# Kernel tuning notes

Hardware: AMD Instinct MI355X
Metric: run time of the kernel (lower is better)

The kernel has to match this reference:

```python
import jax, jax.numpy as jnp
import numpy as np

N = 80         # max_num_nodes
ITERS = 50     # mpm max_iters


def setup_inputs() -> dict:
    key = jax.random.key(0)
    k1, k2 = jax.random.split(key)
    # reconstructed (predicted) adjacency probabilities, kept strictly in (0,1) for BCE
    recon = jax.random.uniform(k1, (N, N), jnp.float32) * 0.98 + 0.01
    # ground-truth binary adjacency, symmetric with self-loops (adj[i,i] used in S build)
    adj = (jax.random.uniform(k2, (N, N), jnp.float32) > 0.5).astype(jnp.float32)
    adj = jnp.maximum(adj, adj.T)
    adj = adj.at[jnp.arange(N), jnp.arange(N)].set(1.0)
    return {"recon_grf": recon, "original_grf": adj}


def _forward(recon, adj):
    # degree-like matching features
    out_features = jnp.sum(recon, axis=1)   # recon node features g_a
    adj_features = jnp.sum(adj, axis=1)     # original node features f_i

    adj_d = jnp.diagonal(adj)               # adj[i,i]
    rec_d = jnp.diagonal(recon)             # recon[a,a]
    eye = jnp.eye(N, dtype=recon.dtype)
    off = 1.0 - eye

    # off-diagonal edge affinities (zero when i==j or a==b, matching the loop skips)
    src = adj * adj_d[:, None] * adj_d[None, :] * off     # [i,j] = adj[i,j]*adj[i,i]*adj[j,j]
    tgt = recon * rec_d[:, None] * rec_d[None, :] * off   # [a,b] = recon[a,b]*recon[a,a]*recon[b,b]

    # diagonal affinities S[i,i,a,a] = adj[i,i]*recon[a,a]*sim(f_i, g_a)
    sim = 1.0 / (jnp.abs(adj_features[:, None] - out_features[None, :]) + 1.0)  # [i,a]
    d = adj_d[:, None] * rec_d[None, :] * sim                                   # [i,a]

    # full affinity tensor S[i,j,a,b]  (N^4 elements)
    S = src[:, :, None, None] * tgt[None, None, :, :] \
        + (eye[:, :, None, None] * eye[None, None, :, :]) * d[:, None, :, None]

    # max-pooling matching (mpm), 50 iterations; checkpoint keeps vjp memory at 1 iter
    @jax.checkpoint
    def step(x):
        # pooled[i,j,a] = max_b x[j,b] * S[i,j,a,b]
        pooled = jnp.max(x[None, :, None, :] * S, axis=3)     # [i,j,a]
        neigh = jnp.sum(pooled * off[:, :, None], axis=1)     # sum over j != i -> [i,a]
        x_new = x * d + neigh                                 # d[i,a] == S[i,i,a,a]
        return x_new / jnp.linalg.norm(x_new)

    x0 = jnp.full((N, N), 1.0 / N, dtype=recon.dtype)
    assignment, _ = jax.lax.scan(lambda x, _: (step(x), None), x0, None, length=ITERS)

    # BCE on the upper triangle (incl. diagonal), mean reduction like F.binary_cross_entropy
    iu = jnp.triu_indices(N)
    t = adj[iu]
    p = recon[iu]
    loss = -jnp.mean(t * jnp.log(p) + (1.0 - t) * jnp.log(1.0 - p))
    return loss, assignment


def reference(recon_grf, original_grf):
    return _forward(recon_grf, original_grf)
```

## Files before the change

### kernel.cpp

```cpp
#include <hip/hip_runtime.h>
#include <math.h>

#define NN 80
#define MITERS 50
#define NTHREADS 1024

typedef _Float16 h8 __attribute__((ext_vector_type(8)));
typedef float f4 __attribute__((ext_vector_type(4)));

__device__ __forceinline__ unsigned pk_mul_f16(unsigned a, unsigned b) {
  unsigned d; asm("v_pk_mul_f16 %0, %1, %2" : "=v"(d) : "v"(a), "v"(b)); return d;
}
__device__ __forceinline__ unsigned pk_max_f16(unsigned a, unsigned b) {
  unsigned d; asm("v_pk_max_f16 %0, %1, %2" : "=v"(d) : "v"(a), "v"(b)); return d;
}
__device__ __forceinline__ h8 as_h8(uint4 u) {
  union { uint4 u; h8 h; } x; x.u = u; return x.h;
}

#define OFF_XH    0
#define OFF_TT    13120
#define OFF_MM0   26240
#define OFF_MM1   42880
#define OFF_SRCH  59520
#define OFF_DLT   76160
#define OFF_FR    103040
#define OFF_FA    103360
#define OFF_RD    103680
#define OFF_AD    104000
#define OFF_WSUM  104320
#define OFF_LSUM  104448
#define LDS_BYTES 104512

#define PB(r, k) ((((r) >> 2) * 656) + (((k) >> 1) * 16) + (((r) & 3) * 4) + (((k) & 1) * 2))

#define DO_TILE(I0, A0, AF)                                                   \
  {                                                                           \
    f4 acc = {0.f, 0.f, 0.f, 0.f};                                            \
    _Pragma("unroll")                                                         \
    for (int ks = 0; ks < 3; ++ks) {                                          \
      const int mo = ((A0) + la) * 208 + ks * 64 + gr * 16;                   \
      const uint4 b0 = *(const uint4*)(MM0b + mo);                            \
      const uint4 b1 = *(const uint4*)(MM1b + mo);                            \
      uint4 bb;                                                               \
      bb.x = pk_max_f16(b0.x, b1.x); bb.y = pk_max_f16(b0.y, b1.y);           \
      bb.z = pk_max_f16(b0.z, b1.z); bb.w = pk_max_f16(b0.w, b1.w);           \
      acc = __builtin_amdgcn_mfma_f32_16x16x32_f16(as_h8(AF[ks]),             \
                                                   as_h8(bb), acc, 0, 0, 0);  \
    }                                                                         \
    const int col = (A0) + la;                                                \
    const int rb = (I0) + gr * 4;                                             \
    const float4 dl = *(const float4*)(DLTb + col * 336 + rb * 4);            \
    char* xa = XHb + (rb >> 2) * 656 + (col >> 1) * 16 + (col & 1) * 2;       \
    const float xo0 = (float)*(const _Float16*)(xa);                          \
    const float xo1 = (float)*(const _Float16*)(xa + 4);                      \
    const float xo2 = (float)*(const _Float16*)(xa + 8);                      \
    const float xo3 = (float)*(const _Float16*)(xa + 12);                     \
    const float n0 = fmaf(xo0, dl.x, acc[0]) * inv;                           \
    const float n1 = fmaf(xo1, dl.y, acc[1]) * inv;                           \
    const float n2 = fmaf(xo2, dl.z, acc[2]) * inv;                           \
    const float n3 = fmaf(xo3, dl.w, acc[3]) * inv;                           \
    ss += n0 * n0 + n1 * n1 + n2 * n2 + n3 * n3;                              \
    *(_Float16*)(xa) = (_Float16)n0;                                          \
    *(_Float16*)(xa + 4) = (_Float16)n1;                                      \
    *(_Float16*)(xa + 8) = (_Float16)n2;                                      \
    *(_Float16*)(xa + 12) = (_Float16)n3;                                     \
  }

__global__ void __launch_bounds__(NTHREADS)
grf_kernel(const float* __restrict__ recon, const float* __restrict__ adj,
           float* __restrict__ out) {
  extern __shared__ char ldsb[];
  char* XHb = ldsb + OFF_XH;
  char* TTb = ldsb + OFF_TT;
  char* MM0b = ldsb + OFF_MM0;
  char* MM1b = ldsb + OFF_MM1;
  char* SRCHb = ldsb + OFF_SRCH;
  char* DLTb = ldsb + OFF_DLT;
  float* FR = (float*)(ldsb + OFF_FR);
  float* FA = (float*)(ldsb + OFF_FA);
  float* RD = (float*)(ldsb + OFF_RD);
  float* AD = (float*)(ldsb + OFF_AD);
  float* WSUM = (float*)(ldsb + OFF_WSUM);
  float* LSUM = (float*)(ldsb + OFF_LSUM);

  const int t = threadIdx.x;
  const int wave = t >> 6, lane = t & 63;
  const int la = lane & 15, gr = lane >> 4;

  if (t < 80) {
    float s = 0.f;
    for (int b = 0; b < NN; ++b) s += recon[t * NN + b];
    FR[t] = s;
    RD[t] = recon[t * NN + t];
  } else if (t < 160) {
    const int i = t - 80;
    float s = 0.f;
    for (int j = 0; j < NN; ++j) s += adj[i * NN + j];
    FA[i] = s;
    AD[i] = adj[i * NN + i];
  }
  if (t < 32) {
    const float q = (float)(_Float16)(1.0f / 80.0f);
    WSUM[t] = (t == 0) ? 6400.0f * q * q : 0.f;
  }
  __syncthreads();

  float lacc = 0.f;
  for (int f = t; f < NN * NN; f += NTHREADS) {
    const int r = f / NN, c = f - (f / NN) * NN;
    *(_Float16*)(XHb + PB(r, c)) = (_Float16)(1.0f / 80.0f);
    const float tv = (r == c) ? 0.f : recon[r * NN + c] * RD[r] * RD[c];
    *(_Float16*)(TTb + PB(r, c)) = (_Float16)tv;
    *(float*)(DLTb + (c * 84 + r) * 4) =
        AD[r] * RD[c] / (fabsf(FA[r] - FR[c]) + 1.f);
    const float sv = (r == c) ? 0.f : adj[r * NN + c] * AD[r] * AD[c];
    *(_Float16*)(SRCHb + (r * 104 + c) * 2) = (_Float16)sv;
    if (c >= r) {
      const float tb = adj[f], p = recon[f];
      lacc -= tb * logf(p) + (1.f - tb) * logf(1.f - p);
    }
  }
  for (int f = t; f < 1920; f += NTHREADS) {
    const int r = f / 24, j = 80 + (f - (f / 24) * 24);
    *(_Float16*)(SRCHb + (r * 104 + j) * 2) = (_Float16)0.f;
  }
  for (int f = t; f < 8320; f += NTHREADS) *(unsigned*)(MM0b + f * 4) = 0u;

  #pragma unroll
  for (int off = 32; off > 0; off >>= 1) lacc += __shfl_down(lacc, off, 64);
  if (lane == 0) LSUM[wave] = lacc;
  __syncthreads();
  if (t == 0) {
    float s = 0.f;
    for (int w = 0; w < 16; ++w) s += LSUM[w];
    out[0] = s / 3240.f;
  }

  const int i00 = (wave / 5) * 16, a00 = (wave % 5) * 16;
  const int tt1 = wave + 16;
  const bool has2 = tt1 < 25;
  const int i01 = has2 ? (tt1 / 5) * 16 : 0;
  const int a01 = has2 ? (tt1 % 5) * 16 : 0;
  uint4 af0[3], af1[3];
  af1[0] = af1[1] = af1[2] = make_uint4(0u, 0u, 0u, 0u);
  #pragma unroll
  for (int ks = 0; ks < 3; ++ks)
    af0[ks] = *(const uint4*)(SRCHb + (i00 + la) * 208 + ks * 64 + gr * 16);
  if (has2) {
    #pragma unroll
    for (int ks = 0; ks < 3; ++ks)
      af1[ks] = *(const uint4*)(SRCHb + (i01 + la) * 208 + ks * 64 + gr * 16);
  }

  const bool actA = t < 800;
  const int g = (t >= 400) ? 1 : 0;
  const int u = g ? t - 400 : t;
  const int rtA = u / 20, ctA = u - (u / 20) * 20;
  const char* xAp = XHb + rtA * 656 + g * 320;
  const char* tAp = TTb + ctA * 656 + g * 320;
  char* mwp = (g ? MM1b : MM0b) + ctA * 4 * 208 + rtA * 8;

  for (int it = 0; it < MITERS; ++it) {
    if (actA) {
      unsigned m[4][4] = {{0u, 0u, 0u, 0u}, {0u, 0u, 0u, 0u},
                          {0u, 0u, 0u, 0u}, {0u, 0u, 0u, 0u}};
      #pragma unroll 4
      for (int cc = 0; cc < 20; ++cc) {
        const uint4 xq = *(const uint4*)(xAp + cc * 16);
        const uint4 tq = *(const uint4*)(tAp + cc * 16);
        const unsigned xr[4] = {xq.x, xq.y, xq.z, xq.w};
        const unsigned tc[4] = {tq.x, tq.y, tq.z, tq.w};
        #pragma unroll
        for (int r = 0; r < 4; ++r)
          #pragma unroll
          for (int c = 0; c < 4; ++c)
            m[r][c] = pk_max_f16(m[r][c], pk_mul_f16(xr[r], tc[c]));
      }
      #pragma unroll
      for (int c = 0; c < 4; ++c) {
        unsigned fr[4];
        #pragma unroll
        for (int r = 0; r < 4; ++r) {
          const unsigned v = m[r][c];
          fr[r] = pk_max_f16(v, (v >> 16) | (v << 16));
        }
        const unsigned w0 = (fr[0] & 0xffffu) | (fr[1] << 16);
        const unsigned w1 = (fr[2] & 0xffffu) | (fr[3] << 16);
        *(uint2*)(mwp + c * 208) = make_uint2(w0, w1);
      }
    }
    __syncthreads();

    const float* WIN = WSUM + ((it & 1) << 4);
    const float4 wa = *(const float4*)(WIN);
    const float4 wb = *(const float4*)(WIN + 4);
    const float4 wc = *(const float4*)(WIN + 8);
    const float4 wd = *(const float4*)(WIN + 12);
    const float tot = ((wa.x + wa.y) + (wa.z + wa.w)) +
                      ((wb.x + wb.y) + (wb.z + wb.w)) +
                      ((wc.x + wc.y) + (wc.z + wc.w)) +
                      ((wd.x + wd.y) + (wd.z + wd.w));
    const float inv = 1.0f / sqrtf(tot);

    float ss = 0.f;
    DO_TILE(i00, a00, af0);
    if (has2) DO_TILE(i01, a01, af1);

    #pragma unroll
    for (int off = 32; off > 0; off >>= 1) ss += __shfl_down(ss, off, 64);
    if (lane == 0) WSUM[(((it + 1) & 1) << 4) + wave] = ss;
    __syncthreads();
  }

  {
    const float* WF = WSUM + ((MITERS & 1) << 4);
    float tot = 0.f;
    #pragma unroll
    for (int w = 0; w < 16; ++w) tot += WF[w];
    const float finv = 1.0f / sqrtf(tot);
    for (int f = t; f < NN * NN; f += NTHREADS) {
      const int i = f / NN, a = f - (f / NN) * NN;
      out[1 + f] = (float)*(const _Float16*)(XHb + PB(i, a)) * finv;
    }
  }
}

extern "C" void kernel_launch(void* const* d_in, const int* in_sizes, int n_in,
                              void* d_out, int out_size, void* d_ws, size_t ws_size,
                              hipStream_t stream) {
  const float* recon = (const float*)d_in[0];
  const float* adj   = (const float*)d_in[1];
  float* out = (float*)d_out;
  (void)in_sizes; (void)n_in; (void)out_size; (void)d_ws; (void)ws_size;

  hipFuncSetAttribute(reinterpret_cast<const void*>(grf_kernel),
                      hipFuncAttributeMaxDynamicSharedMemorySize, LDS_BYTES);
  grf_kernel<<<1, NTHREADS, LDS_BYTES, stream>>>(recon, adj, out);
}
```

Measured before the change: 364.4 us.

## Split max-pool phase four ways, cache target tile in registers, keep x in fp32 regs

The max-pooling phase now splits the b dimension into four groups of 256 threads (800 active threads in total, versus 800 across two halves before). Each thread covers an 8-row by 4-col tile over 10 b-chunks and holds its target-matrix slice in registers across all iterations. The MFMA stage max-reduces four partial buffers instead of two, and the LDS footprint grows to hold them. Each thread also keeps its own previous x values in fp32 registers instead of rereading fp16 from LDS, which removes some LDS traffic. The costs are higher register pressure and larger LDS use.

```diff
diff --git a/kernel.cpp b/kernel.cpp
--- a/kernel.cpp
+++ b/kernel.cpp
@@ -20,47 +20,47 @@
 
 #define OFF_XH    0
 #define OFF_TT    13120
-#define OFF_MM0   26240
-#define OFF_MM1   42880
-#define OFF_SRCH  59520
-#define OFF_DLT   76160
-#define OFF_FR    103040
-#define OFF_FA    103360
-#define OFF_RD    103680
-#define OFF_AD    104000
-#define OFF_WSUM  104320
-#define OFF_LSUM  104448
-#define LDS_BYTES 104512
+#define OFF_MM    26240
+#define OFF_SRCH  92800
+#define OFF_DLT   109440
+#define OFF_FR    136320
+#define OFF_FA    136640
+#define OFF_RD    136960
+#define OFF_AD    137280
+#define OFF_WSUM  137600
+#define OFF_LSUM  137728
+#define LDS_BYTES 137792
 
 #define PB(r, k) ((((r) >> 2) * 656) + (((k) >> 1) * 16) + (((r) & 3) * 4) + (((k) & 1) * 2))
 
-#define DO_TILE(I0, A0, AF)                                                   \
+#define DO_TILE(I0, A0, AF, XO)                                               \
   {                                                                           \
     f4 acc = {0.f, 0.f, 0.f, 0.f};                                            \
     _Pragma("unroll")                                                         \
     for (int ks = 0; ks < 3; ++ks) {                                          \
       const int mo = ((A0) + la) * 208 + ks * 64 + gr * 16;                   \
-      const uint4 b0 = *(const uint4*)(MM0b + mo);                            \
-      const uint4 b1 = *(const uint4*)(MM1b + mo);                            \
+      const uint4 b0 = *(const uint4*)(MMb + mo);                             \
+      const uint4 b1 = *(const uint4*)(MMb + 16640 + mo);                     \
+      const uint4 b2 = *(const uint4*)(MMb + 33280 + mo);                     \
+      const uint4 b3 = *(const uint4*)(MMb + 49920 + mo);                     \
       uint4 bb;                                                               \
-      bb.x = pk_max_f16(b0.x, b1.x); bb.y = pk_max_f16(b0.y, b1.y);           \
-      bb.z = pk_max_f16(b0.z, b1.z); bb.w = pk_max_f16(b0.w, b1.w);           \
+      bb.x = pk_max_f16(pk_max_f16(b0.x, b1.x), pk_max_f16(b2.x, b3.x));      \
+      bb.y = pk_max_f16(pk_max_f16(b0.y, b1.y), pk_max_f16(b2.y, b3.y));      \
+      bb.z = pk_max_f16(pk_max_f16(b0.z, b1.z), pk_max_f16(b2.z, b3.z));      \
+      bb.w = pk_max_f16(pk_max_f16(b0.w, b1.w), pk_max_f16(b2.w, b3.w));      \
       acc = __builtin_amdgcn_mfma_f32_16x16x32_f16(as_h8(AF[ks]),             \
                                                    as_h8(bb), acc, 0, 0, 0);  \
     }                                                                         \
     const int col = (A0) + la;                                                \
     const int rb = (I0) + gr * 4;                                             \
     const float4 dl = *(const float4*)(DLTb + col * 336 + rb * 4);            \
-    char* xa = XHb + (rb >> 2) * 656 + (col >> 1) * 16 + (col & 1) * 2;       \
-    const float xo0 = (float)*(const _Float16*)(xa);                          \
-    const float xo1 = (float)*(const _Float16*)(xa + 4);                      \
-    const float xo2 = (float)*(const _Float16*)(xa + 8);                      \
-    const float xo3 = (float)*(const _Float16*)(xa + 12);                     \
-    const float n0 = fmaf(xo0, dl.x, acc[0]) * inv;                           \
-    const float n1 = fmaf(xo1, dl.y, acc[1]) * inv;                           \
-    const float n2 = fmaf(xo2, dl.z, acc[2]) * inv;                           \
-    const float n3 = fmaf(xo3, dl.w, acc[3]) * inv;                           \
+    const float n0 = fmaf(XO[0], dl.x, acc[0]) * inv;                         \
+    const float n1 = fmaf(XO[1], dl.y, acc[1]) * inv;                         \
+    const float n2 = fmaf(XO[2], dl.z, acc[2]) * inv;                         \
+    const float n3 = fmaf(XO[3], dl.w, acc[3]) * inv;                         \
     ss += n0 * n0 + n1 * n1 + n2 * n2 + n3 * n3;                              \
+    XO[0] = n0; XO[1] = n1; XO[2] = n2; XO[3] = n3;                           \
+    char* xa = XHb + (((I0) >> 2) + gr) * 656 + (col >> 1) * 16 + (col & 1) * 2; \
     *(_Float16*)(xa) = (_Float16)n0;                                          \
     *(_Float16*)(xa + 4) = (_Float16)n1;                                      \
     *(_Float16*)(xa + 8) = (_Float16)n2;                                      \
@@ -73,8 +73,7 @@
   extern __shared__ char ldsb[];
   char* XHb = ldsb + OFF_XH;
   char* TTb = ldsb + OFF_TT;
-  char* MM0b = ldsb + OFF_MM0;
-  char* MM1b = ldsb + OFF_MM1;
+  char* MMb = ldsb + OFF_MM;
   char* SRCHb = ldsb + OFF_SRCH;
   char* DLTb = ldsb + OFF_DLT;
   float* FR = (float*)(ldsb + OFF_FR);
@@ -125,7 +124,7 @@
     const int r = f / 24, j = 80 + (f - (f / 24) * 24);
     *(_Float16*)(SRCHb + (r * 104 + j) * 2) = (_Float16)0.f;
   }
-  for (int f = t; f < 8320; f += NTHREADS) *(unsigned*)(MM0b + f * 4) = 0u;
+  for (int f = t; f < 16640; f += NTHREADS) *(unsigned*)(MMb + f * 4) = 0u;
 
   #pragma unroll
   for (int off = 32; off > 0; off >>= 1) lacc += __shfl_down(lacc, off, 64);
@@ -153,41 +152,53 @@
       af1[ks] = *(const uint4*)(SRCHb + (i01 + la) * 208 + ks * 64 + gr * 16);
   }
 
-  const bool actA = t < 800;
-  const int g = (t >= 400) ? 1 : 0;
-  const int u = g ? t - 400 : t;
-  const int rtA = u / 20, ctA = u - (u / 20) * 20;
-  const char* xAp = XHb + rtA * 656 + g * 320;
-  const char* tAp = TTb + ctA * 656 + g * 320;
-  char* mwp = (g ? MM1b : MM0b) + ctA * 4 * 208 + rtA * 8;
+  const int g = t >> 8;
+  const int u = t & 255;
+  const bool actA = (u < 200);
+  const int rtA = u / 20;
+  const int ctA = u - rtA * 20;
+  const char* xbase = XHb + (2 * rtA) * 656 + g * 160;
+  char* mwp = MMb + g * 16640 + (ctA * 4) * 208 + rtA * 16;
+
+  uint4 tr[10];
+  #pragma unroll
+  for (int cc = 0; cc < 10; ++cc)
+    tr[cc] = *(const uint4*)(TTb + ctA * 656 + (g * 10 + cc) * 16);
+
+  float xo0[4], xo1[4];
+  #pragma unroll
+  for (int k = 0; k < 4; ++k) xo0[k] = xo1[k] = (float)(_Float16)(1.0f / 80.0f);
 
   for (int it = 0; it < MITERS; ++it) {
     if (actA) {
-      unsigned m[4][4] = {{0u, 0u, 0u, 0u}, {0u, 0u, 0u, 0u},
-                          {0u, 0u, 0u, 0u}, {0u, 0u, 0u, 0u}};
-      #pragma unroll 4
-      for (int cc = 0; cc < 20; ++cc) {
-        const uint4 xq = *(const uint4*)(xAp + cc * 16);
-        const uint4 tq = *(const uint4*)(tAp + cc * 16);
-        const unsigned xr[4] = {xq.x, xq.y, xq.z, xq.w};
-        const unsigned tc[4] = {tq.x, tq.y, tq.z, tq.w};
+      unsigned m[8][4];
+      #pragma unroll
+      for (int r = 0; r < 8; ++r)
         #pragma unroll
-        for (int r = 0; r < 4; ++r)
+        for (int c = 0; c < 4; ++c) m[r][c] = 0u;
+      #pragma unroll 2
+      for (int cc = 0; cc < 10; ++cc) {
+        const uint4 x0 = *(const uint4*)(xbase + cc * 16);
+        const uint4 x1 = *(const uint4*)(xbase + 656 + cc * 16);
+        const unsigned xr[8] = {x0.x, x0.y, x0.z, x0.w, x1.x, x1.y, x1.z, x1.w};
+        const unsigned tc[4] = {tr[cc].x, tr[cc].y, tr[cc].z, tr[cc].w};
+        #pragma unroll
+        for (int r = 0; r < 8; ++r)
           #pragma unroll
           for (int c = 0; c < 4; ++c)
             m[r][c] = pk_max_f16(m[r][c], pk_mul_f16(xr[r], tc[c]));
       }
       #pragma unroll
       for (int c = 0; c < 4; ++c) {
-        unsigned fr[4];
+        unsigned lo[8];
         #pragma unroll
-        for (int r = 0; r < 4; ++r) {
+        for (int r = 0; r < 8; ++r) {
           const unsigned v = m[r][c];
-          fr[r] = pk_max_f16(v, (v >> 16) | (v << 16));
+          lo[r] = pk_max_f16(v, (v >> 16) | (v << 16)) & 0xffffu;
         }
-        const unsigned w0 = (fr[0] & 0xffffu) | (fr[1] << 16);
-        const unsigned w1 = (fr[2] & 0xffffu) | (fr[3] << 16);
-        *(uint2*)(mwp + c * 208) = make_uint2(w0, w1);
+        const uint4 w = make_uint4(lo[0] | (lo[1] << 16), lo[2] | (lo[3] << 16),
+                                   lo[4] | (lo[5] << 16), lo[6] | (lo[7] << 16));
+        *(uint4*)(mwp + c * 208) = w;
       }
     }
     __syncthreads();
@@ -204,8 +215,8 @@
     const float inv = 1.0f / sqrtf(tot);
 
     float ss = 0.f;
-    DO_TILE(i00, a00, af0);
-    if (has2) DO_TILE(i01, a01, af1);
+    DO_TILE(i00, a00, af0, xo0);
+    if (has2) DO_TILE(i01, a01, af1, xo1);
 
     #pragma unroll
     for (int off = 32; off > 0; off >>= 1) ss += __shfl_down(ss, off, 64);
```

New measurement: 444.4 us. +22.0%, slower.
